# Optimization experiments

Hardware: AMD Instinct MI355X
Metric: run time of the kernel (lower is better)

The kernel has to match this reference:

```python
import jax, jax.numpy as jnp
import numpy as np

D_MODEL = 768
D_STATE = 16
D_CONV = 4
EXPAND = 2
D_INNER = EXPAND * D_MODEL          # 1536
DT_RANK = (D_MODEL + 15) // 16      # 48 (mamba default: ceil(d_model/16))


def setup_inputs() -> dict:
    key = jax.random.key(0)
    ks = jax.random.split(key, 8)
    B, T = 2, 1024
    s = 0.02
    return {
        "x": jax.random.normal(ks[0], (B, T, D_MODEL), jnp.float32),
        "ln_g": jnp.ones((D_MODEL,), jnp.float32),
        "ln_b": jnp.zeros((D_MODEL,), jnp.float32),
        "W_in": jax.random.normal(ks[1], (2 * D_INNER, D_MODEL), jnp.float32) * s,
        "conv_w": jax.random.normal(ks[2], (D_INNER, 1, D_CONV), jnp.float32) * s,
        "conv_b": jnp.zeros((D_INNER,), jnp.float32),
        "W_xproj": jax.random.normal(ks[3], (DT_RANK + 2 * D_STATE, D_INNER), jnp.float32) * s,
        "W_dt": jax.random.normal(ks[4], (D_INNER, DT_RANK), jnp.float32) * s,
        "b_dt": jax.random.normal(ks[5], (D_INNER,), jnp.float32) * s,
        "A_log": jnp.log(jnp.broadcast_to(jnp.arange(1.0, D_STATE + 1.0, dtype=jnp.float32), (D_INNER, D_STATE))),
        "Dp": jnp.ones((D_INNER,), jnp.float32),
        "W_out": jax.random.normal(ks[6], (D_MODEL, D_INNER), jnp.float32) * s,
    }


def _mamba_block(x, ln_g, ln_b, W_in, conv_w, conv_b, W_xproj, W_dt, b_dt, A_log, Dp, W_out):
    B, T, D = x.shape
    # LayerNorm
    mu = x.mean(-1, keepdims=True)
    var = ((x - mu) ** 2).mean(-1, keepdims=True)
    h = (x - mu) * jax.lax.rsqrt(var + 1e-5) * ln_g + ln_b
    # in_proj -> [B,T,2*d_inner], split into x-branch and gate z
    xz = h @ W_in.T
    xs, z = jnp.split(xz, 2, axis=-1)
    # causal depthwise conv over time (pad left d_conv-1), then SiLU
    xc = jax.lax.conv_general_dilated(
        xs.transpose(0, 2, 1), conv_w, (1,), [(D_CONV - 1, 0)],
        dimension_numbers=("NCH", "OIH", "NCH"), feature_group_count=D_INNER)
    xc = jax.nn.silu(xc.transpose(0, 2, 1) + conv_b)  # [B,T,d_inner]
    # x_proj -> dt_rank + 2*d_state
    x_dbl = xc @ W_xproj.T
    dt_r = x_dbl[..., :DT_RANK]
    Bm = x_dbl[..., DT_RANK:DT_RANK + D_STATE]       # [B,T,n]
    Cm = x_dbl[..., DT_RANK + D_STATE:]              # [B,T,n]
    dt = jax.nn.softplus(dt_r @ W_dt.T + b_dt)       # [B,T,d_inner]
    A = -jnp.exp(A_log)                              # [d_inner, n]
    dA = jnp.exp(jnp.einsum("btd,dn->btdn", dt, A))  # [B,T,d,n]
    dBu = jnp.einsum("btd,btn->btdn", dt * xc, Bm)   # [B,T,d,n]

    def step(s, inp):
        dA_t, dBu_t, C_t = inp
        s = dA_t * s + dBu_t                          # [B,d,n]
        y_t = jnp.einsum("bdn,bn->bd", s, C_t)
        return s, y_t

    s0 = jnp.zeros((B, D_INNER, D_STATE), x.dtype)
    _, ys = jax.lax.scan(step, s0,
                         (dA.transpose(1, 0, 2, 3), dBu.transpose(1, 0, 2, 3), Cm.transpose(1, 0, 2)))
    y = ys.transpose(1, 0, 2) + Dp * xc              # D skip connection
    y = y * jax.nn.silu(z)                           # gate
    return x + y @ W_out.T                           # out_proj + residual


def reference(x, ln_g, ln_b, W_in, conv_w, conv_b, W_xproj, W_dt, b_dt, A_log, Dp, W_out):
    return _mamba_block(x, ln_g, ln_b, W_in, conv_w, conv_b, W_xproj, W_dt, b_dt, A_log, Dp, W_out)
```

## Files before the change

kernel.cpp:

```cpp
#include <hip/hip_runtime.h>

typedef unsigned short u16;
typedef unsigned int u32;
typedef __attribute__((ext_vector_type(8))) short short8;
typedef __attribute__((ext_vector_type(4))) float f32x4;

#define D_MODEL 768
#define D_INNER 1536
#define D_XZ    3072
#define D_STATE 16
#define DT_RANK 48
#define NROW    2048
#define SEQ     1024
#define XDS     128
#define NCHUNK  128
#define CLEN    8

typedef const __attribute__((address_space(1))) u32 glb_u32;
typedef __attribute__((address_space(3))) u32 lds_u32;

__device__ __forceinline__ float bf2f(u16 u) {
    union { unsigned int i; float f; } v; v.i = ((unsigned int)u) << 16; return v.f;
}
__device__ __forceinline__ u16 f2bf(float f) {
    union { float f; unsigned int i; } v; v.f = f;
    unsigned int r = v.i + 0x7fffu + ((v.i >> 16) & 1u);
    return (u16)(r >> 16);
}
__device__ __forceinline__ void g2lds16(const u16* g, u16* l) {
    __builtin_amdgcn_global_load_lds((glb_u32*)g, (lds_u32*)l, 16, 0, 0);
}

#define N0 (D_XZ * D_MODEL / 4)
#define N1 (D_MODEL * D_INNER / 4)
#define N2 (XDS * D_INNER / 4)
#define N3 (D_INNER * 64 / 4)
#define N4 (D_INNER * D_STATE / 4)
#define N5 (NROW * XDS / 4)
#define PREP_BLOCKS ((N0+N1+N2+N3+N4+N5) / 256)
__global__ __launch_bounds__(256) void prep_ln_k(
    const float* __restrict__ x, const float* __restrict__ g,
    const float* __restrict__ bln, u16* __restrict__ h,
    const float* __restrict__ W_in, const float* __restrict__ W_out,
    const float* __restrict__ W_xp, const float* __restrict__ W_dt,
    const float* __restrict__ A_log,
    u16* __restrict__ Win_bf, u16* __restrict__ Wout_bf,
    u16* __restrict__ Wxp_bf, u16* __restrict__ Wdt_bf,
    float* __restrict__ negA, float* __restrict__ xdbl)
{
    __shared__ float sred[4], sqred[4];
    int tid = threadIdx.x;
    if (blockIdx.x < NROW) {
        int row = blockIdx.x;
        const float* xr = x + (size_t)row * D_MODEL;
        float v[3], s = 0.f, sq = 0.f;
#pragma unroll
        for (int j = 0; j < 3; ++j) {
            v[j] = xr[tid + j * 256];
            s += v[j]; sq += v[j] * v[j];
        }
#pragma unroll
        for (int off = 32; off >= 1; off >>= 1) {
            s  += __shfl_xor(s,  off, 64);
            sq += __shfl_xor(sq, off, 64);
        }
        if ((tid & 63) == 0) { sred[tid >> 6] = s; sqred[tid >> 6] = sq; }
        __syncthreads();
        float st = sred[0] + sred[1] + sred[2] + sred[3];
        float sqt = sqred[0] + sqred[1] + sqred[2] + sqred[3];
        float mu = st * (1.f / D_MODEL);
        float var = sqt * (1.f / D_MODEL) - mu * mu;
        float rstd = rsqrtf(var + 1e-5f);
        u16* hr = h + (size_t)row * D_MODEL;
#pragma unroll
        for (int j = 0; j < 3; ++j) {
            int idx = tid + j * 256;
            hr[idx] = f2bf((v[j] - mu) * rstd * g[idx] + bln[idx]);
        }
        return;
    }
    int gid = (blockIdx.x - NROW) * 256 + tid;
    if (gid < N0) {
        float4 v = *(const float4*)(W_in + (size_t)gid * 4);
        u16* o = Win_bf + (size_t)gid * 4;
        o[0]=f2bf(v.x); o[1]=f2bf(v.y); o[2]=f2bf(v.z); o[3]=f2bf(v.w);
    } else if (gid < N0 + N1) {
        int i = gid - N0;
        float4 v = *(const float4*)(W_out + (size_t)i * 4);
        u16* o = Wout_bf + (size_t)i * 4;
        o[0]=f2bf(v.x); o[1]=f2bf(v.y); o[2]=f2bf(v.z); o[3]=f2bf(v.w);
    } else if (gid < N0 + N1 + N2) {
        int i = gid - N0 - N1;
        int n = (i * 4) / D_INNER, k = (i * 4) % D_INNER;
        u16* o = Wxp_bf + (size_t)i * 4;
        if (n < 80) {
            float4 v = *(const float4*)(W_xp + (size_t)n * D_INNER + k);
            o[0]=f2bf(v.x); o[1]=f2bf(v.y); o[2]=f2bf(v.z); o[3]=f2bf(v.w);
        } else { o[0]=0; o[1]=0; o[2]=0; o[3]=0; }
    } else if (gid < N0 + N1 + N2 + N3) {
        int i = gid - N0 - N1 - N2;
        int r = (i * 4) >> 6, c0 = (i * 4) & 63;
        u16* o = Wdt_bf + (size_t)i * 4;
        if (c0 < DT_RANK) {
            float4 v = *(const float4*)(W_dt + (size_t)r * DT_RANK + c0);
            o[0]=f2bf(v.x); o[1]=f2bf(v.y); o[2]=f2bf(v.z); o[3]=f2bf(v.w);
        } else { o[0]=0; o[1]=0; o[2]=0; o[3]=0; }
    } else if (gid < N0 + N1 + N2 + N3 + N4) {
        int i = gid - N0 - N1 - N2 - N3;
        float4 v = *(const float4*)(A_log + (size_t)i * 4);
        *(float4*)(negA + (size_t)i * 4) =
            make_float4(-__expf(v.x), -__expf(v.y), -__expf(v.z), -__expf(v.w));
    } else if (gid < N0 + N1 + N2 + N3 + N4 + N5) {
        int i = gid - N0 - N1 - N2 - N3 - N4;
        *(float4*)(xdbl + (size_t)i * 4) = make_float4(0.f, 0.f, 0.f, 0.f);
    }
}

template<int MT, int NT, bool OUT_BF16, bool ADD_RES>
__global__ __launch_bounds__(256) void gemm128(
    const u16* __restrict__ A, const u16* __restrict__ B,
    const float* __restrict__ Res, void* __restrict__ Cv,
    int M, int N, int K)
{
    constexpr int BM = 32 * MT, BN = 32 * NT;
    __shared__ __align__(16) u16 As[BM * 32];
    __shared__ __align__(16) u16 Bs[BN * 32];
    int tid = threadIdx.x, w = tid >> 6, lane = tid & 63;
    int wm = w & 1, wn = w >> 1;
    int m0 = blockIdx.x * BM, n0 = blockIdx.y * BN;
    int mloc = lane & 15, quad = lane >> 4;
    int lr = lane >> 2, lc = lane & 3;
    f32x4 acc[MT][NT] = {};

    for (int k0 = 0; k0 < K; k0 += 32) {
        __syncthreads();
#pragma unroll
        for (int j = w; j < 2 * MT; j += 4) {
            int row = j * 16 + lr;
            int cb = lc ^ ((row >> 1) & 3);
            g2lds16(A + (size_t)(m0 + row) * K + k0 + cb * 8, &As[j * 512]);
        }
#pragma unroll
        for (int j = w; j < 2 * NT; j += 4) {
            int row = j * 16 + lr;
            int cb = lc ^ ((row >> 1) & 3);
            g2lds16(B + (size_t)(n0 + row) * K + k0 + cb * 8, &Bs[j * 512]);
        }
        __syncthreads();
        short8 afr[MT], bfr[NT];
#pragma unroll
        for (int mt = 0; mt < MT; ++mt) {
            int row = wm * MT * 16 + mt * 16 + mloc;
            int cb = quad ^ ((row >> 1) & 3);
            afr[mt] = *(const short8*)(&As[row * 32 + cb * 8]);
        }
#pragma unroll
        for (int nt = 0; nt < NT; ++nt) {
            int row = wn * NT * 16 + nt * 16 + mloc;
            int cb = quad ^ ((row >> 1) & 3);
            bfr[nt] = *(const short8*)(&Bs[row * 32 + cb * 8]);
        }
#pragma unroll
        for (int mt = 0; mt < MT; ++mt)
#pragma unroll
            for (int nt = 0; nt < NT; ++nt)
                acc[mt][nt] = __builtin_amdgcn_mfma_f32_16x16x32_bf16(
                    afr[mt], bfr[nt], acc[mt][nt], 0, 0, 0);
    }
#pragma unroll
    for (int mt = 0; mt < MT; ++mt) {
        int grow0 = m0 + wm * MT * 16 + mt * 16 + quad * 4;
#pragma unroll
        for (int nt = 0; nt < NT; ++nt) {
            int gcol = n0 + wn * NT * 16 + nt * 16 + mloc;
#pragma unroll
            for (int r = 0; r < 4; ++r) {
                size_t idx = (size_t)(grow0 + r) * N + gcol;
                float v = acc[mt][nt][r];
                if (ADD_RES) v += Res[idx];
                if (OUT_BF16) ((u16*)Cv)[idx] = f2bf(v);
                else          ((float*)Cv)[idx] = v;
            }
        }
    }
}

template<int MT, int NT, int KSLICE>
__global__ __launch_bounds__(256) void gemm_splitk(
    const u16* __restrict__ A, const u16* __restrict__ B,
    float* __restrict__ Cout, int K, int CS)
{
    constexpr int BM = 32 * MT, BN = 32 * NT;
    __shared__ __align__(16) u16 As[BM * 32];
    __shared__ __align__(16) u16 Bs[BN * 32];
    int tid = threadIdx.x, w = tid >> 6, lane = tid & 63;
    int wm = w & 1, wn = w >> 1;
    int m0 = blockIdx.x * BM, n0 = blockIdx.y * BN;
    int kbase = blockIdx.z * KSLICE;
    int mloc = lane & 15, quad = lane >> 4;
    int lr = lane >> 2, lc = lane & 3;
    f32x4 acc[MT][NT] = {};

    for (int k0 = 0; k0 < KSLICE; k0 += 32) {
        __syncthreads();
#pragma unroll
        for (int j = w; j < 2 * MT; j += 4) {
            int row = j * 16 + lr;
            int cb = lc ^ ((row >> 1) & 3);
            g2lds16(A + (size_t)(m0 + row) * K + kbase + k0 + cb * 8, &As[j * 512]);
        }
#pragma unroll
        for (int j = w; j < 2 * NT; j += 4) {
            int row = j * 16 + lr;
            int cb = lc ^ ((row >> 1) & 3);
            g2lds16(B + (size_t)(n0 + row) * K + kbase + k0 + cb * 8, &Bs[j * 512]);
        }
        __syncthreads();
        short8 afr[MT], bfr[NT];
#pragma unroll
        for (int mt = 0; mt < MT; ++mt) {
            int row = wm * MT * 16 + mt * 16 + mloc;
            int cb = quad ^ ((row >> 1) & 3);
            afr[mt] = *(const short8*)(&As[row * 32 + cb * 8]);
        }
#pragma unroll
        for (int nt = 0; nt < NT; ++nt) {
            int row = wn * NT * 16 + nt * 16 + mloc;
            int cb = quad ^ ((row >> 1) & 3);
            bfr[nt] = *(const short8*)(&Bs[row * 32 + cb * 8]);
        }
#pragma unroll
        for (int mt = 0; mt < MT; ++mt)
#pragma unroll
            for (int nt = 0; nt < NT; ++nt)
                acc[mt][nt] = __builtin_amdgcn_mfma_f32_16x16x32_bf16(
                    afr[mt], bfr[nt], acc[mt][nt], 0, 0, 0);
    }
#pragma unroll
    for (int mt = 0; mt < MT; ++mt) {
        int grow0 = m0 + wm * MT * 16 + mt * 16 + quad * 4;
#pragma unroll
        for (int nt = 0; nt < NT; ++nt) {
            int gcol = n0 + wn * NT * 16 + nt * 16 + mloc;
#pragma unroll
            for (int r = 0; r < 4; ++r)
                unsafeAtomicAdd(&Cout[(size_t)(grow0 + r) * CS + gcol],
                                acc[mt][nt][r]);
        }
    }
}

__global__ __launch_bounds__(256) void dtgemm_k(
    const float* __restrict__ xdbl, const u16* __restrict__ Wdt,
    const float* __restrict__ bias, u16* __restrict__ dtout)
{
    __shared__ __align__(16) u16 Bs[64 * 72];
    int tid = threadIdx.x, wave = tid >> 6, lane = tid & 63;
    int m0 = blockIdx.x * 64, n0 = blockIdx.y * 64;
    int mloc = lane & 15, quad = lane >> 4;
    {
        int r = tid >> 3, ck = (tid & 7) * 8;
#pragma unroll
        for (int rr = 0; rr < 64; rr += 32) {
            int4 bv = *(const int4*)(Wdt + (size_t)(n0 + r + rr) * 64 + ck);
            *(int4*)(&Bs[(r + rr) * 72 + ck]) = bv;
        }
    }
    int arow = m0 + wave * 16 + mloc;
    const float* ar = xdbl + (size_t)arow * XDS + quad * 8;
    short8 af[2];
#pragma unroll
    for (int h = 0; h < 2; ++h) {
        float4 a0 = *(const float4*)(ar + h * 32);
        float4 a1 = *(const float4*)(ar + h * 32 + 4);
        short8 t;
        t[0]=(short)f2bf(a0.x); t[1]=(short)f2bf(a0.y);
        t[2]=(short)f2bf(a0.z); t[3]=(short)f2bf(a0.w);
        t[4]=(short)f2bf(a1.x); t[5]=(short)f2bf(a1.y);
        t[6]=(short)f2bf(a1.z); t[7]=(short)f2bf(a1.w);
        af[h] = t;
    }
    __syncthreads();
    f32x4 acc[4] = {};
#pragma unroll
    for (int h = 0; h < 2; ++h)
#pragma unroll
        for (int nt = 0; nt < 4; ++nt) {
            short8 bf = *(const short8*)(&Bs[(nt * 16 + mloc) * 72 + h * 32 + quad * 8]);
            acc[nt] = __builtin_amdgcn_mfma_f32_16x16x32_bf16(af[h], bf, acc[nt], 0, 0, 0);
        }
#pragma unroll
    for (int nt = 0; nt < 4; ++nt) {
        int gcol = n0 + nt * 16 + mloc;
        int grow = m0 + wave * 16 + quad * 4;
#pragma unroll
        for (int r = 0; r < 4; ++r) {
            float t = acc[nt][r] + bias[gcol];
            float sp = (t > 15.f) ? t : __logf(1.f + __expf(t));
            dtout[(size_t)(grow + r) * D_INNER + gcol] = f2bf(sp);
        }
    }
}

__global__ __launch_bounds__(256) void conv_silu_k(
    const u16* __restrict__ xz, const float* __restrict__ cw,
    const float* __restrict__ cb, u16* __restrict__ xc)
{
    int gid = blockIdx.x * 256 + threadIdx.x;
    int r = gid / (D_INNER / 4);
    int c4 = (gid - r * (D_INNER / 4)) * 4;
    int t = r & (SEQ - 1);
    float4 cbv = *(const float4*)(cb + c4);
    float acc[4] = {cbv.x, cbv.y, cbv.z, cbv.w};
    float4 wv[4];
#pragma unroll
    for (int j = 0; j < 4; ++j) wv[j] = *(const float4*)(cw + (c4 + j) * 4);
#pragma unroll
    for (int k = 0; k < 4; ++k) {
        int tt = t - 3 + k;
        if (tt >= 0) {
            ushort4 xv = *(const ushort4*)(xz + (size_t)(r - 3 + k) * D_XZ + c4);
            acc[0] += bf2f(xv.x) * ((const float*)&wv[0])[k];
            acc[1] += bf2f(xv.y) * ((const float*)&wv[1])[k];
            acc[2] += bf2f(xv.z) * ((const float*)&wv[2])[k];
            acc[3] += bf2f(xv.w) * ((const float*)&wv[3])[k];
        }
    }
    ushort4 o;
    o.x = f2bf(acc[0] / (1.f + __expf(-acc[0])));
    o.y = f2bf(acc[1] / (1.f + __expf(-acc[1])));
    o.z = f2bf(acc[2] / (1.f + __expf(-acc[2])));
    o.w = f2bf(acc[3] / (1.f + __expf(-acc[3])));
    *(ushort4*)(xc + (size_t)r * D_INNER + c4) = o;
}

__global__ __launch_bounds__(256) void scan_p1(
    const u16* __restrict__ dt, const u16* __restrict__ xc,
    const float* __restrict__ xdbl, const float* __restrict__ negA,
    float* __restrict__ Sbuf, float* __restrict__ dtsumbuf)
{
    __shared__ float Bsh[CLEN][D_STATE];
    int tid = threadIdx.x;
    int gid = blockIdx.x * 256 + tid;
    int d = gid % D_INNER;
    int bcN = gid / D_INNER;
    int c = bcN % NCHUNK, b = bcN / NCHUNK;
    size_t r0 = (size_t)b * SEQ + c * CLEN;
    if (tid < CLEN * D_STATE) {
        int tt = tid >> 4, n = tid & 15;
        Bsh[tt][n] = xdbl[(r0 + tt) * XDS + DT_RANK + n];
    }
    float a[D_STATE], s[D_STATE] = {};
    {
        const float4* Ar = (const float4*)(negA + d * D_STATE);
        float4 a0 = Ar[0], a1 = Ar[1], a2 = Ar[2], a3 = Ar[3];
        a[0]=a0.x; a[1]=a0.y; a[2]=a0.z; a[3]=a0.w;
        a[4]=a1.x; a[5]=a1.y; a[6]=a1.z; a[7]=a1.w;
        a[8]=a2.x; a[9]=a2.y; a[10]=a2.z; a[11]=a2.w;
        a[12]=a3.x; a[13]=a3.y; a[14]=a3.z; a[15]=a3.w;
    }
    float dtv[CLEN], du[CLEN];
    const u16* dp = dt + r0 * D_INNER + d;
    const u16* xp = xc + r0 * D_INNER + d;
#pragma unroll
    for (int t = 0; t < CLEN; ++t) {
        dtv[t] = bf2f(dp[t * D_INNER]);
        du[t] = dtv[t] * bf2f(xp[t * D_INNER]);
    }
    __syncthreads();
    float dtsum = 0.f;
#pragma unroll
    for (int t = 0; t < CLEN; ++t) {
        dtsum += dtv[t];
#pragma unroll
        for (int n = 0; n < D_STATE; ++n)
            s[n] = __expf(dtv[t] * a[n]) * s[n] + du[t] * Bsh[t][n];
    }
    float4* So = (float4*)(Sbuf + (size_t)gid * D_STATE);
#pragma unroll
    for (int j = 0; j < 4; ++j)
        So[j] = make_float4(s[j*4], s[j*4+1], s[j*4+2], s[j*4+3]);
    dtsumbuf[gid] = dtsum;
}

__global__ __launch_bounds__(256) void scan_p2(
    const float* __restrict__ Sbuf, const float* __restrict__ dtsumbuf,
    const float* __restrict__ negA, float* __restrict__ carry)
{
    int gid = blockIdx.x * 256 + threadIdx.x;
    int n = gid % D_STATE;
    int d = (gid / D_STATE) % D_INNER;
    int b = gid / (D_STATE * D_INNER);
    float a = negA[d * D_STATE + n];
    float s = 0.f;
#pragma unroll 8
    for (int c = 0; c < NCHUNK; ++c) {
        size_t idx = ((size_t)(b * NCHUNK + c) * D_INNER + d);
        carry[idx * D_STATE + n] = s;
        s = Sbuf[idx * D_STATE + n] + __expf(a * dtsumbuf[idx]) * s;
    }
}

__global__ __launch_bounds__(256) void scan_p3(
    const u16* __restrict__ dt, const u16* __restrict__ xc,
    const u16* __restrict__ xz, const float* __restrict__ xdbl,
    const float* __restrict__ negA, const float* __restrict__ Dp,
    const float* __restrict__ carry, u16* __restrict__ yy)
{
    __shared__ float BCsh[CLEN][2 * D_STATE];
    int tid = threadIdx.x;
    int gid = blockIdx.x * 256 + tid;
    int d = gid % D_INNER;
    int bcN = gid / D_INNER;
    int c = bcN % NCHUNK, b = bcN / NCHUNK;
    size_t r0 = (size_t)b * SEQ + c * CLEN;
    {
        int tt = tid >> 5, j = tid & 31;
        BCsh[tt][j] = xdbl[(r0 + tt) * XDS + DT_RANK + j];
    }
    float a[D_STATE], s[D_STATE];
    {
        const float4* Ci = (const float4*)(carry + (size_t)gid * D_STATE);
        float4 c0 = Ci[0], c1 = Ci[1], c2 = Ci[2], c3 = Ci[3];
        s[0]=c0.x; s[1]=c0.y; s[2]=c0.z; s[3]=c0.w;
        s[4]=c1.x; s[5]=c1.y; s[6]=c1.z; s[7]=c1.w;
        s[8]=c2.x; s[9]=c2.y; s[10]=c2.z; s[11]=c2.w;
        s[12]=c3.x; s[13]=c3.y; s[14]=c3.z; s[15]=c3.w;
        const float4* Ar = (const float4*)(negA + d * D_STATE);
        float4 a0 = Ar[0], a1 = Ar[1], a2 = Ar[2], a3 = Ar[3];
        a[0]=a0.x; a[1]=a0.y; a[2]=a0.z; a[3]=a0.w;
        a[4]=a1.x; a[5]=a1.y; a[6]=a1.z; a[7]=a1.w;
        a[8]=a2.x; a[9]=a2.y; a[10]=a2.z; a[11]=a2.w;
        a[12]=a3.x; a[13]=a3.y; a[14]=a3.z; a[15]=a3.w;
    }
    float dtv[CLEN], xcv[CLEN], zv[CLEN];
    const u16* dp = dt + r0 * D_INNER + d;
    const u16* xp = xc + r0 * D_INNER + d;
    const u16* zp = xz + r0 * D_XZ + D_INNER + d;
#pragma unroll
    for (int t = 0; t < CLEN; ++t) {
        dtv[t] = bf2f(dp[t * D_INNER]);
        xcv[t] = bf2f(xp[t * D_INNER]);
        zv[t]  = bf2f(zp[t * D_XZ]);
    }
    float dpv = Dp[d];
    __syncthreads();
    u16* yp = yy + r0 * D_INNER + d;
#pragma unroll
    for (int t = 0; t < CLEN; ++t) {
        float du = dtv[t] * xcv[t];
        float y = 0.f;
#pragma unroll
        for (int n = 0; n < D_STATE; ++n) {
            s[n] = __expf(dtv[t] * a[n]) * s[n] + du * BCsh[t][n];
            y += s[n] * BCsh[t][D_STATE + n];
        }
        float yv = y + dpv * xcv[t];
        float sig = 1.f / (1.f + __expf(-zv[t]));
        yp[t * D_INNER] = f2bf(yv * (zv[t] * sig));
    }
}

extern "C" void kernel_launch(void* const* d_in, const int* in_sizes, int n_in,
                              void* d_out, int out_size, void* d_ws, size_t ws_size,
                              hipStream_t stream) {
    const float* x      = (const float*)d_in[0];
    const float* ln_g   = (const float*)d_in[1];
    const float* ln_b   = (const float*)d_in[2];
    const float* W_in   = (const float*)d_in[3];
    const float* conv_w = (const float*)d_in[4];
    const float* conv_b = (const float*)d_in[5];
    const float* W_xp   = (const float*)d_in[6];
    const float* W_dt   = (const float*)d_in[7];
    const float* b_dt   = (const float*)d_in[8];
    const float* A_log  = (const float*)d_in[9];
    const float* Dp     = (const float*)d_in[10];
    const float* W_out  = (const float*)d_in[11];
    float* out = (float*)d_out;

    char* ws = (char*)d_ws;
    u16*   h_bf    = (u16*)ws;   ws += (size_t)NROW * D_MODEL * 2;
    u16*   xz_bf   = (u16*)ws;   ws += (size_t)NROW * D_XZ * 2;
    u16*   xc_bf   = (u16*)ws;   ws += (size_t)NROW * D_INNER * 2;
    float* xdbl    = (float*)ws; ws += (size_t)NROW * XDS * 4;
    u16*   dtbuf   = (u16*)ws;   ws += (size_t)NROW * D_INNER * 2;
    u16*   yybuf   = (u16*)ws;   ws += (size_t)NROW * D_INNER * 2;
    u16*   Win_bf  = (u16*)ws;   ws += (size_t)D_XZ * D_MODEL * 2;
    u16*   Wout_bf = (u16*)ws;   ws += (size_t)D_MODEL * D_INNER * 2;
    u16*   Wxp_bf  = (u16*)ws;   ws += (size_t)XDS * D_INNER * 2;
    u16*   Wdt_bf  = (u16*)ws;   ws += (size_t)D_INNER * 64 * 2;
    float* negA    = (float*)ws; ws += (size_t)D_INNER * D_STATE * 4;
    float* Sbuf    = (float*)ws; ws += (size_t)2 * NCHUNK * D_INNER * 16 * 4;
    float* dtsumb  = (float*)ws; ws += (size_t)2 * NCHUNK * D_INNER * 4;
    float* carryb  = (float*)ws;

    prep_ln_k<<<NROW + PREP_BLOCKS, 256, 0, stream>>>(
        x, ln_g, ln_b, h_bf, W_in, W_out, W_xp, W_dt, A_log,
        Win_bf, Wout_bf, Wxp_bf, Wdt_bf, negA, xdbl);

    gemm128<4, 2, true, false><<<dim3(NROW / 128, D_XZ / 64), 256, 0, stream>>>(
        h_bf, Win_bf, nullptr, xz_bf, NROW, D_XZ, D_MODEL);
    conv_silu_k<<<NROW * (D_INNER / 4) / 256, 256, 0, stream>>>(
        xz_bf, conv_w, conv_b, xc_bf);
    gemm_splitk<2, 4, 192><<<dim3(NROW / 64, 1, 8), 256, 0, stream>>>(
        xc_bf, Wxp_bf, xdbl, D_INNER, XDS);
    dtgemm_k<<<dim3(NROW / 64, D_INNER / 64), 256, 0, stream>>>(
        xdbl, Wdt_bf, b_dt, dtbuf);

    scan_p1<<<2 * NCHUNK * D_INNER / 256, 256, 0, stream>>>(
        dtbuf, xc_bf, xdbl, negA, Sbuf, dtsumb);
    scan_p2<<<2 * D_INNER * D_STATE / 256, 256, 0, stream>>>(
        Sbuf, dtsumb, negA, carryb);
    scan_p3<<<2 * NCHUNK * D_INNER / 256, 256, 0, stream>>>(
        dtbuf, xc_bf, xz_bf, xdbl, negA, Dp, carryb, yybuf);

    gemm128<2, 2, false, true><<<dim3(NROW / 64, D_MODEL / 64), 256, 0, stream>>>(
        yybuf, Wout_bf, x, out, NROW, D_MODEL, D_INNER);
}
```

Measured before the change: 203.7 us.

## Store chunked scan states in bf16 and double chunk length

Halves the number of scan chunks by doubling chunk length from 8 to 16. This shrinks the per-chunk state buffers and the length of the sequential carry pass. The intermediate chunk states and carries are now stored as bf16 instead of fp32, which halves memory traffic between the three scan phases. The trade-offs are lower precision in the carried state and a longer serial loop per thread in phases 1 and 3.

```diff
diff --git a/kernel.cpp b/kernel.cpp
--- a/kernel.cpp
+++ b/kernel.cpp
@@ -3,6 +3,7 @@
 typedef unsigned short u16;
 typedef unsigned int u32;
 typedef __attribute__((ext_vector_type(8))) short short8;
+typedef __attribute__((ext_vector_type(8))) unsigned short ushort8;
 typedef __attribute__((ext_vector_type(4))) float f32x4;
 
 #define D_MODEL 768
@@ -13,8 +14,8 @@
 #define NROW    2048
 #define SEQ     1024
 #define XDS     128
-#define NCHUNK  128
-#define CLEN    8
+#define NCHUNK  64
+#define CLEN    16
 
 typedef const __attribute__((address_space(1))) u32 glb_u32;
 typedef __attribute__((address_space(3))) u32 lds_u32;
@@ -337,7 +338,7 @@
 __global__ __launch_bounds__(256) void scan_p1(
     const u16* __restrict__ dt, const u16* __restrict__ xc,
     const float* __restrict__ xdbl, const float* __restrict__ negA,
-    float* __restrict__ Sbuf, float* __restrict__ dtsumbuf)
+    u16* __restrict__ Sbuf, float* __restrict__ dtsumbuf)
 {
     __shared__ float Bsh[CLEN][D_STATE];
     int tid = threadIdx.x;
@@ -346,7 +347,7 @@
     int bcN = gid / D_INNER;
     int c = bcN % NCHUNK, b = bcN / NCHUNK;
     size_t r0 = (size_t)b * SEQ + c * CLEN;
-    if (tid < CLEN * D_STATE) {
+    {
         int tt = tid >> 4, n = tid & 15;
         Bsh[tt][n] = xdbl[(r0 + tt) * XDS + DT_RANK + n];
     }
@@ -376,16 +377,17 @@
         for (int n = 0; n < D_STATE; ++n)
             s[n] = __expf(dtv[t] * a[n]) * s[n] + du[t] * Bsh[t][n];
     }
-    float4* So = (float4*)(Sbuf + (size_t)gid * D_STATE);
-#pragma unroll
-    for (int j = 0; j < 4; ++j)
-        So[j] = make_float4(s[j*4], s[j*4+1], s[j*4+2], s[j*4+3]);
+    ushort8 so[2];
+#pragma unroll
+    for (int j = 0; j < 16; ++j) so[j >> 3][j & 7] = f2bf(s[j]);
+    *(ushort8*)(Sbuf + (size_t)gid * D_STATE) = so[0];
+    *(ushort8*)(Sbuf + (size_t)gid * D_STATE + 8) = so[1];
     dtsumbuf[gid] = dtsum;
 }
 
 __global__ __launch_bounds__(256) void scan_p2(
-    const float* __restrict__ Sbuf, const float* __restrict__ dtsumbuf,
-    const float* __restrict__ negA, float* __restrict__ carry)
+    const u16* __restrict__ Sbuf, const float* __restrict__ dtsumbuf,
+    const float* __restrict__ negA, u16* __restrict__ carry)
 {
     int gid = blockIdx.x * 256 + threadIdx.x;
     int n = gid % D_STATE;
@@ -396,8 +398,8 @@
 #pragma unroll 8
     for (int c = 0; c < NCHUNK; ++c) {
         size_t idx = ((size_t)(b * NCHUNK + c) * D_INNER + d);
-        carry[idx * D_STATE + n] = s;
-        s = Sbuf[idx * D_STATE + n] + __expf(a * dtsumbuf[idx]) * s;
+        carry[idx * D_STATE + n] = f2bf(s);
+        s = bf2f(Sbuf[idx * D_STATE + n]) + __expf(a * dtsumbuf[idx]) * s;
     }
 }
 
@@ -405,7 +407,7 @@
     const u16* __restrict__ dt, const u16* __restrict__ xc,
     const u16* __restrict__ xz, const float* __restrict__ xdbl,
     const float* __restrict__ negA, const float* __restrict__ Dp,
-    const float* __restrict__ carry, u16* __restrict__ yy)
+    const u16* __restrict__ carry, u16* __restrict__ yy)
 {
     __shared__ float BCsh[CLEN][2 * D_STATE];
     int tid = threadIdx.x;
@@ -414,18 +416,18 @@
     int bcN = gid / D_INNER;
     int c = bcN % NCHUNK, b = bcN / NCHUNK;
     size_t r0 = (size_t)b * SEQ + c * CLEN;
-    {
-        int tt = tid >> 5, j = tid & 31;
-        BCsh[tt][j] = xdbl[(r0 + tt) * XDS + DT_RANK + j];
+#pragma unroll
+    for (int j = 0; j < 2; ++j) {
+        int idx = tid + j * 256;
+        int row = idx >> 5, col = idx & 31;
+        BCsh[row][col] = xdbl[(r0 + row) * XDS + DT_RANK + col];
     }
     float a[D_STATE], s[D_STATE];
     {
-        const float4* Ci = (const float4*)(carry + (size_t)gid * D_STATE);
-        float4 c0 = Ci[0], c1 = Ci[1], c2 = Ci[2], c3 = Ci[3];
-        s[0]=c0.x; s[1]=c0.y; s[2]=c0.z; s[3]=c0.w;
-        s[4]=c1.x; s[5]=c1.y; s[6]=c1.z; s[7]=c1.w;
-        s[8]=c2.x; s[9]=c2.y; s[10]=c2.z; s[11]=c2.w;
-        s[12]=c3.x; s[13]=c3.y; s[14]=c3.z; s[15]=c3.w;
+        ushort8 c0 = *(const ushort8*)(carry + (size_t)gid * D_STATE);
+        ushort8 c1 = *(const ushort8*)(carry + (size_t)gid * D_STATE + 8);
+#pragma unroll
+        for (int j = 0; j < 8; ++j) { s[j] = bf2f(c0[j]); s[8 + j] = bf2f(c1[j]); }
         const float4* Ar = (const float4*)(negA + d * D_STATE);
         float4 a0 = Ar[0], a1 = Ar[1], a2 = Ar[2], a3 = Ar[3];
         a[0]=a0.x; a[1]=a0.y; a[2]=a0.z; a[3]=a0.w;
@@ -490,9 +492,9 @@
     u16*   Wxp_bf  = (u16*)ws;   ws += (size_t)XDS * D_INNER * 2;
     u16*   Wdt_bf  = (u16*)ws;   ws += (size_t)D_INNER * 64 * 2;
     float* negA    = (float*)ws; ws += (size_t)D_INNER * D_STATE * 4;
-    float* Sbuf    = (float*)ws; ws += (size_t)2 * NCHUNK * D_INNER * 16 * 4;
+    u16*   Sbuf    = (u16*)ws;   ws += (size_t)2 * NCHUNK * D_INNER * 16 * 2;
     float* dtsumb  = (float*)ws; ws += (size_t)2 * NCHUNK * D_INNER * 4;
-    float* carryb  = (float*)ws;
+    u16*   carryb  = (u16*)ws;
 
     prep_ln_k<<<NROW + PREP_BLOCKS, 256, 0, stream>>>(
         x, ln_g, ln_b, h_bf, W_in, W_out, W_xp, W_dt, A_log,
```

Measured after the change: 194.7 us. -4.4%, faster.
